# Kernel optimization log

Measured on AMD Instinct MI355X. Metric: run time of the kernel, lower is better.

The kernel has to match this reference:

```python
import jax, jax.numpy as jnp
import numpy as np

N_E = 4096
E_DIM = 256


def setup_inputs() -> dict:
    key = jax.random.key(0)
    k1, k2 = jax.random.split(key)
    z = jax.random.normal(k1, (32, 2048, E_DIM), dtype=jnp.float32)
    # nn.Embedding weight initialized uniform(-1/n_e, 1/n_e)
    codebook = jax.random.uniform(k2, (N_E, E_DIM), dtype=jnp.float32,
                                  minval=-1.0 / N_E, maxval=1.0 / N_E)
    return {"z": z, "codebook": codebook}


def reference(z, codebook):
    # z: [B, T, e_dim], codebook: [n_e, e_dim]
    z_flat = z.reshape(-1, z.shape[-1])                      # [N, d]
    # squared euclidean distance: ||z||^2 + ||e||^2 - 2 z.e^T
    d = (jnp.sum(z_flat ** 2, axis=1, keepdims=True)
         + jnp.sum(codebook ** 2, axis=1)
         - 2.0 * jnp.einsum('nd,kd->nk', z_flat, codebook))  # [N, n_e]
    idx = jnp.argmin(d, axis=1)                              # [N]
    z_q = codebook[idx].reshape(z.shape)                     # [B, T, d]
    return z_q
```

## Files before the change

### kernel.cpp

```cpp
#include <hip/hip_runtime.h>
#include <hip/hip_fp16.h>
#include <cfloat>
#include <climits>

#define D     256
#define NE    4096
#define MT    64
#define NSPLITB 8
#define DELTA     1.5e-4f
#define CAND_CAP  131072

typedef _Float16 f16x8 __attribute__((ext_vector_type(8)));
typedef __attribute__((ext_vector_type(4))) float f32x4;

#define SYNC(n) do { \
    asm volatile("s_waitcnt vmcnt(" #n ")\n\ts_barrier" ::: "memory"); \
    __builtin_amdgcn_sched_barrier(0); \
} while (0)

__device__ __forceinline__ float np_block128_sq(const float* __restrict__ p) {
    float r[8];
    #pragma unroll
    for (int j = 0; j < 8; ++j) r[j] = __fmul_rn(p[j], p[j]);
    #pragma unroll
    for (int i = 8; i < 128; i += 8)
        #pragma unroll
        for (int j = 0; j < 8; ++j) r[j] = __fadd_rn(r[j], __fmul_rn(p[i + j], p[i + j]));
    return __fadd_rn(__fadd_rn(__fadd_rn(r[0], r[1]), __fadd_rn(r[2], r[3])),
                     __fadd_rn(__fadd_rn(r[4], r[5]), __fadd_rn(r[6], r[7])));
}
__device__ __forceinline__ float np_sumsq256(const float* __restrict__ p) {
    return __fadd_rn(np_block128_sq(p), np_block128_sq(p + 128));
}
__device__ __forceinline__ float np_einsum_dot256(const float* __restrict__ zr,
                                                  const float* __restrict__ er) {
    float v0 = 0.f, v1 = 0.f, v2 = 0.f, v3 = 0.f;
    for (int t = 0; t < 256; t += 16) {
        float4 a0 = *(const float4*)(zr + t);
        float4 a1 = *(const float4*)(zr + t + 4);
        float4 a2 = *(const float4*)(zr + t + 8);
        float4 a3 = *(const float4*)(zr + t + 12);
        float4 b0 = *(const float4*)(er + t);
        float4 b1 = *(const float4*)(er + t + 4);
        float4 b2 = *(const float4*)(er + t + 8);
        float4 b3 = *(const float4*)(er + t + 12);
        v0 = __fadd_rn(v0, __fmul_rn(a3.x, b3.x));
        v1 = __fadd_rn(v1, __fmul_rn(a3.y, b3.y));
        v2 = __fadd_rn(v2, __fmul_rn(a3.z, b3.z));
        v3 = __fadd_rn(v3, __fmul_rn(a3.w, b3.w));
        v0 = __fadd_rn(v0, __fmul_rn(a2.x, b2.x));
        v1 = __fadd_rn(v1, __fmul_rn(a2.y, b2.y));
        v2 = __fadd_rn(v2, __fmul_rn(a2.z, b2.z));
        v3 = __fadd_rn(v3, __fmul_rn(a2.w, b2.w));
        v0 = __fadd_rn(v0, __fmul_rn(a1.x, b1.x));
        v1 = __fadd_rn(v1, __fmul_rn(a1.y, b1.y));
        v2 = __fadd_rn(v2, __fmul_rn(a1.z, b1.z));
        v3 = __fadd_rn(v3, __fmul_rn(a1.w, b1.w));
        v0 = __fadd_rn(v0, __fmul_rn(a0.x, b0.x));
        v1 = __fadd_rn(v1, __fmul_rn(a0.y, b0.y));
        v2 = __fadd_rn(v2, __fmul_rn(a0.z, b0.z));
        v3 = __fadd_rn(v3, __fmul_rn(a0.w, b0.w));
    }
    return __fadd_rn(__fadd_rn(v0, v1), __fadd_rn(v2, v3));
}

__global__ void bnp_kernel(const float* __restrict__ cb, float* __restrict__ Bnp) {
    int k = blockIdx.x * 256 + threadIdx.x;
    if (k < NE) Bnp[k] = np_sumsq256(cb + (size_t)k * D);
}

__global__ void tof16_kernel(const float* __restrict__ x,
                             unsigned short* __restrict__ y, float scale, int n4) {
    int t = blockIdx.x * 256 + threadIdx.x;
    if (t >= n4) return;
    float4 v = *(const float4*)(x + (size_t)t * 4);
    ushort4 o;
    o.x = __half_as_ushort(__float2half_rn(v.x * scale));
    o.y = __half_as_ushort(__float2half_rn(v.y * scale));
    o.z = __half_as_ushort(__float2half_rn(v.z * scale));
    o.w = __half_as_ushort(__float2half_rn(v.w * scale));
    *(ushort4*)(y + (size_t)t * 4) = o;
}

__device__ __forceinline__ void gload_lds16(const void* g, void* l) {
    __builtin_amdgcn_global_load_lds(
        (const __attribute__((address_space(1))) unsigned int*)g,
        (__attribute__((address_space(3))) unsigned int*)l, 16, 0, 0);
}

__global__ __launch_bounds__(256, 2)
void stageA_f16(const float* __restrict__ z,
                const unsigned short* __restrict__ cb2,
                const float* __restrict__ Bnp, int* __restrict__ idxArr,
                float* __restrict__ rowMin, unsigned long long* __restrict__ rowKey,
                int* __restrict__ flagCnt, int* __restrict__ flagList) {
    __shared__ unsigned char lds[16384 + 4 * 8192];
    float* BnpL = (float*)lds;
    unsigned short* Bt = (unsigned short*)(lds + 16384);

    const int tid  = threadIdx.x;
    const int wid  = tid >> 6;
    const int lane = tid & 63;
    const int ln   = lane & 15;
    const int qd   = lane >> 4;
    const int wn   = wid;
    const int R0   = blockIdx.x * MT;

    #pragma unroll
    for (int i = 0; i < 4; ++i) {
        int j = tid + 256 * i;
        *(float4*)(BnpL + j * 4) = *(const float4*)(Bnp + j * 4);
    }

    f16x8 fa[8][4];
    {
        const float* za = z + (size_t)(R0 + ln) * 256 + qd * 8;
        #pragma unroll
        for (int kc = 0; kc < 8; ++kc)
            #pragma unroll
            for (int mt = 0; mt < 4; ++mt) {
                const float* p = za + mt * 16 * 256 + kc * 32;
                float4 a = *(const float4*)p, b = *(const float4*)(p + 4);
                f16x8 h;
                h[0] = (_Float16)a.x; h[1] = (_Float16)a.y;
                h[2] = (_Float16)a.z; h[3] = (_Float16)a.w;
                h[4] = (_Float16)b.x; h[5] = (_Float16)b.y;
                h[6] = (_Float16)b.z; h[7] = (_Float16)b.w;
                fa[kc][mt] = h;
            }
    }

    const int cA  = wid * 32 + (lane >> 2);
    const int sgA = (lane & 3) ^ ((cA >> 1) & 3);
    const unsigned short* srcA = cb2 + cA * 256 + sgA * 8;
    unsigned short* dstW = Bt + wid * 1024;
    const int boffs = ((wn * 32 + ln) << 6) + ((qd ^ ((ln >> 1) & 3)) << 4);
    const unsigned char* btb = (const unsigned char*)Bt;

    float best1[16], best2[16];
    int   bidx[16];
    #pragma unroll
    for (int i = 0; i < 16; ++i) { best1[i] = FLT_MAX; best2[i] = FLT_MAX; bidx[i] = 0; }

    #pragma unroll
    for (int s = 0; s < 3; ++s) {
        gload_lds16(srcA + s * 32, dstW + s * 4096);
        gload_lds16(srcA + s * 32 + 4096, dstW + s * 4096 + 512);
    }
    __syncthreads();

    for (int ct = 0; ct < 31; ++ct) {
        f32x4 acc[4][2];
        #pragma unroll
        for (int i = 0; i < 4; ++i)
            #pragma unroll
            for (int j = 0; j < 2; ++j) acc[i][j] = (f32x4){0.f, 0.f, 0.f, 0.f};

        #pragma unroll
        for (int kc = 0; kc < 8; ++kc) {
            SYNC(4);
            {
                const int s3k = kc + 3;
                int off = (ct + (s3k >> 3)) * 32768 + (s3k & 7) * 32;
                unsigned short* d = dstW + ((s3k & 3) << 12);
                gload_lds16(srcA + off, d);
                gload_lds16(srcA + off + 4096, d + 512);
            }
            f16x8 fb[2];
            #pragma unroll
            for (int nt = 0; nt < 2; ++nt)
                fb[nt] = *(const f16x8*)(btb + ((kc & 3) << 13) + boffs + nt * 1024);
            __builtin_amdgcn_s_setprio(1);
            #pragma unroll
            for (int mt = 0; mt < 4; ++mt)
                #pragma unroll
                for (int nt = 0; nt < 2; ++nt)
                    acc[mt][nt] = __builtin_amdgcn_mfma_f32_16x16x32_f16(
                        fa[kc][mt], fb[nt], acc[mt][nt], 0, 0, 0);
            __builtin_amdgcn_s_setprio(0);

            if (kc == 7) {
                const int C0 = ct * 128;
                #pragma unroll
                for (int nt = 0; nt < 2; ++nt) {
                    int col = C0 + wn * 32 + nt * 16 + ln;
                    float bn = BnpL[col];
                    #pragma unroll
                    for (int mt = 0; mt < 4; ++mt) {
                        f32x4 a = acc[mt][nt];
                        #pragma unroll
                        for (int r = 0; r < 4; ++r) {
                            float s = fmaf(-4.8828125e-4f, a[r], bn);
                            int ii = mt * 4 + r;
                            bool lt = s < best1[ii];
                            best2[ii] = __builtin_amdgcn_fmed3f(best1[ii], best2[ii], s);
                            bidx[ii]  = lt ? col : bidx[ii];
                            best1[ii] = fminf(best1[ii], s);
                        }
                    }
                }
            }
        }
    }
    {
        const int ct = 31;
        f32x4 acc[4][2];
        #pragma unroll
        for (int i = 0; i < 4; ++i)
            #pragma unroll
            for (int j = 0; j < 2; ++j) acc[i][j] = (f32x4){0.f, 0.f, 0.f, 0.f};

        #pragma unroll
        for (int kc = 0; kc < 8; ++kc) {
            if (kc <= 5) { SYNC(4); } else if (kc == 6) { SYNC(2); } else { SYNC(0); }
            if (kc <= 4) {
                const int s3k = kc + 3;
                int off = ct * 32768 + (s3k & 7) * 32;
                unsigned short* d = dstW + ((s3k & 3) << 12);
                gload_lds16(srcA + off, d);
                gload_lds16(srcA + off + 4096, d + 512);
            }
            f16x8 fb[2];
            #pragma unroll
            for (int nt = 0; nt < 2; ++nt)
                fb[nt] = *(const f16x8*)(btb + ((kc & 3) << 13) + boffs + nt * 1024);
            __builtin_amdgcn_s_setprio(1);
            #pragma unroll
            for (int mt = 0; mt < 4; ++mt)
                #pragma unroll
                for (int nt = 0; nt < 2; ++nt)
                    acc[mt][nt] = __builtin_amdgcn_mfma_f32_16x16x32_f16(
                        fa[kc][mt], fb[nt], acc[mt][nt], 0, 0, 0);
            __builtin_amdgcn_s_setprio(0);

            if (kc == 7) {
                const int C0 = ct * 128;
                #pragma unroll
                for (int nt = 0; nt < 2; ++nt) {
                    int col = C0 + wn * 32 + nt * 16 + ln;
                    float bn = BnpL[col];
                    #pragma unroll
                    for (int mt = 0; mt < 4; ++mt) {
                        f32x4 a = acc[mt][nt];
                        #pragma unroll
                        for (int r = 0; r < 4; ++r) {
                            float s = fmaf(-4.8828125e-4f, a[r], bn);
                            int ii = mt * 4 + r;
                            bool lt = s < best1[ii];
                            best2[ii] = __builtin_amdgcn_fmed3f(best1[ii], best2[ii], s);
                            bidx[ii]  = lt ? col : bidx[ii];
                            best1[ii] = fminf(best1[ii], s);
                        }
                    }
                }
            }
        }
    }

    #pragma unroll
    for (int mask = 1; mask < 16; mask <<= 1) {
        #pragma unroll
        for (int ii = 0; ii < 16; ++ii) {
            float c1 = __shfl_xor(best1[ii], mask);
            float c2 = __shfl_xor(best2[ii], mask);
            int   ci = __shfl_xor(bidx[ii], mask);
            if (c1 < best1[ii] || (c1 == best1[ii] && ci < bidx[ii])) {
                best2[ii] = fminf(best1[ii], c2);
                best1[ii] = c1; bidx[ii] = ci;
            } else {
                best2[ii] = fminf(best2[ii], c1);
            }
        }
    }
    __syncthreads();
    float* mb1 = (float*)lds;
    float* mb2 = mb1 + 256;
    int*   mix = (int*)(mb2 + 256);
    if (ln == 0) {
        #pragma unroll
        for (int mt = 0; mt < 4; ++mt)
            #pragma unroll
            for (int r = 0; r < 4; ++r) {
                int row = mt * 16 + qd * 4 + r;
                mb1[row * 4 + wn] = best1[mt * 4 + r];
                mb2[row * 4 + wn] = best2[mt * 4 + r];
                mix[row * 4 + wn] = bidx[mt * 4 + r];
            }
    }
    __syncthreads();
    if (tid < MT) {
        int r = tid;
        float b1 = mb1[r * 4], b2v = mb2[r * 4]; int ix = mix[r * 4];
        #pragma unroll
        for (int w = 1; w < 4; ++w) {
            float c1 = mb1[r * 4 + w], c2 = mb2[r * 4 + w]; int ci = mix[r * 4 + w];
            if (c1 < b1 || (c1 == b1 && ci < ix)) { b2v = fminf(b1, c2); b1 = c1; ix = ci; }
            else b2v = fminf(b2v, c1);
        }
        idxArr[R0 + r] = ix;
        rowMin[R0 + r] = b1;
        rowKey[R0 + r] = ~0ULL;
        if (b2v - b1 <= DELTA) {
            int p = atomicAdd(flagCnt, 1);
            flagList[p] = R0 + r;
        }
    }
}

__global__ __launch_bounds__(256, 2)
void stageB_f16(const float* __restrict__ z,
                const unsigned short* __restrict__ cb2,
                const float* __restrict__ Bnp, const float* __restrict__ rowMin,
                const int* __restrict__ flagCnt, const int* __restrict__ flagList,
                int* __restrict__ candCnt, unsigned int* __restrict__ candList) {
    __shared__ unsigned char lds[4 * 8192 + 512];
    unsigned short* Bt = (unsigned short*)lds;
    int*   frow   = (int*)(lds + 32768);
    float* rmin_l = (float*)(lds + 32768 + 256);

    const int nf = *flagCnt;
    const int R0 = blockIdx.x * MT;
    if (R0 >= nf) return;
    const int m = min(MT, nf - R0);

    const int tid  = threadIdx.x;
    const int wid  = tid >> 6;
    const int lane = tid & 63;
    const int ln   = lane & 15;
    const int qd   = lane >> 4;
    const int wn   = wid;
    const int ktBeg = blockIdx.y * (NE / NSPLITB);

    if (tid < MT) {
        int fr = flagList[R0 + min(tid, m - 1)];
        frow[tid] = fr;
        rmin_l[tid] = rowMin[fr];
    }
    __syncthreads();

    float rmv[16];
    #pragma unroll
    for (int mt = 0; mt < 4; ++mt)
        #pragma unroll
        for (int r = 0; r < 4; ++r)
            rmv[mt * 4 + r] = rmin_l[mt * 16 + qd * 4 + r];

    float bnv[4][2];
    #pragma unroll
    for (int ct = 0; ct < 4; ++ct)
        #pragma unroll
        for (int nt = 0; nt < 2; ++nt)
            bnv[ct][nt] = Bnp[ktBeg + ct * 128 + wn * 32 + nt * 16 + ln];

    f16x8 fa[8][4];
    {
        int rA[4];
        #pragma unroll
        for (int mt = 0; mt < 4; ++mt) rA[mt] = frow[mt * 16 + ln];
        #pragma unroll
        for (int kc = 0; kc < 8; ++kc)
            #pragma unroll
            for (int mt = 0; mt < 4; ++mt) {
                const float* p = z + (size_t)rA[mt] * 256 + kc * 32 + qd * 8;
                float4 a = *(const float4*)p, b = *(const float4*)(p + 4);
                f16x8 h;
                h[0] = (_Float16)a.x; h[1] = (_Float16)a.y;
                h[2] = (_Float16)a.z; h[3] = (_Float16)a.w;
                h[4] = (_Float16)b.x; h[5] = (_Float16)b.y;
                h[6] = (_Float16)b.z; h[7] = (_Float16)b.w;
                fa[kc][mt] = h;
            }
    }

    const int cA  = wid * 32 + (lane >> 2);
    const int sgA = (lane & 3) ^ ((cA >> 1) & 3);
    const unsigned short* srcA = cb2 + (size_t)(ktBeg + cA) * 256 + sgA * 8;
    unsigned short* dstW = Bt + wid * 1024;
    const int boffs = ((wn * 32 + ln) << 6) + ((qd ^ ((ln >> 1) & 3)) << 4);
    const unsigned char* btb = (const unsigned char*)Bt;

    #pragma unroll
    for (int s = 0; s < 3; ++s) {
        gload_lds16(srcA + s * 32, dstW + s * 4096);
        gload_lds16(srcA + s * 32 + 4096, dstW + s * 4096 + 512);
    }
    __syncthreads();

    unsigned long long hm0 = 0, hm1 = 0;

    #pragma unroll
    for (int ct = 0; ct < 4; ++ct) {
        f32x4 acc[4][2];
        #pragma unroll
        for (int i = 0; i < 4; ++i)
            #pragma unroll
            for (int j = 0; j < 2; ++j) acc[i][j] = (f32x4){0.f, 0.f, 0.f, 0.f};

        #pragma unroll
        for (int kc = 0; kc < 8; ++kc) {
            const int s = ct * 8 + kc;
            if (s <= 29) { SYNC(4); } else if (s == 30) { SYNC(2); } else { SYNC(0); }
            if (s <= 28) {
                const int s3 = s + 3;
                int off = (s3 >> 3) * 32768 + (s3 & 7) * 32;
                unsigned short* d = dstW + ((s3 & 3) << 12);
                gload_lds16(srcA + off, d);
                gload_lds16(srcA + off + 4096, d + 512);
            }
            f16x8 fb[2];
            #pragma unroll
            for (int nt = 0; nt < 2; ++nt)
                fb[nt] = *(const f16x8*)(btb + ((s & 3) << 13) + boffs + nt * 1024);
            __builtin_amdgcn_s_setprio(1);
            #pragma unroll
            for (int mt = 0; mt < 4; ++mt)
                #pragma unroll
                for (int nt = 0; nt < 2; ++nt)
                    acc[mt][nt] = __builtin_amdgcn_mfma_f32_16x16x32_f16(
                        fa[kc][mt], fb[nt], acc[mt][nt], 0, 0, 0);
            __builtin_amdgcn_s_setprio(0);

            if (kc == 7) {
                #pragma unroll
                for (int nt = 0; nt < 2; ++nt)
                    #pragma unroll
                    for (int mt = 0; mt < 4; ++mt) {
                        f32x4 a = acc[mt][nt];
                        #pragma unroll
                        for (int r = 0; r < 4; ++r) {
                            float sc = fmaf(-4.8828125e-4f, a[r], bnv[ct][nt]);
                            if (sc <= rmv[mt * 4 + r] + DELTA) {
                                unsigned long long bit =
                                    1ull << (((ct & 1) << 5) | (nt << 4) | (mt << 2) | r);
                                if (ct < 2) hm0 |= bit; else hm1 |= bit;
                            }
                        }
                    }
            }
        }
    }

    #pragma unroll
    for (int h = 0; h < 2; ++h) {
        unsigned long long hm = h ? hm1 : hm0;
        while (hm) {
            int b = __builtin_ctzll(hm);
            hm &= hm - 1;
            int ctb = h * 2 + (b >> 5);
            int ntb = (b >> 4) & 1, mtb = (b >> 2) & 3, rb = b & 3;
            int col = ktBeg + ctb * 128 + wn * 32 + ntb * 16 + ln;
            int row = frow[mtb * 16 + qd * 4 + rb];
            int p = atomicAdd(candCnt, 1);
            if (p < CAND_CAP)
                candList[p] = ((unsigned)row << 12) | (unsigned)col;
        }
    }
}

__global__ void stageC(const float* __restrict__ z, const float* __restrict__ cb,
                       const float* __restrict__ Bnp,
                       const int* __restrict__ candCnt,
                       const unsigned int* __restrict__ candList,
                       unsigned long long* __restrict__ rowKey) {
    int c = blockIdx.x * 256 + threadIdx.x;
    int n = min(*candCnt, CAND_CAP);
    if (c >= n) return;
    unsigned e = candList[c];
    int r = (int)(e >> 12);
    int k = (int)(e & 4095u);
    float Anp = np_sumsq256(z + (size_t)r * D);
    float C   = np_einsum_dot256(z + (size_t)r * D, cb + (size_t)k * D);
    float AB  = __fadd_rn(Anp, Bnp[k]);
    float s   = __fsub_rn(AB, __fadd_rn(C, C));
    unsigned long long key = ((unsigned long long)__float_as_uint(s) << 32) | (unsigned)k;
    atomicMin(rowKey + r, key);
}

__global__ void gather_kernel(const float* __restrict__ cb,
                              const int* __restrict__ idxArr,
                              const unsigned long long* __restrict__ rowKey,
                              float* __restrict__ out) {
    int r = blockIdx.x * 4 + (threadIdx.x >> 6);
    int l = threadIdx.x & 63;
    unsigned long long kv = rowKey[r];
    int ix = (kv != ~0ULL) ? (int)(kv & 0xFFFFFFFFull) : idxArr[r];
    *(float4*)(out + (size_t)r * D + l * 4) =
        *(const float4*)(cb + (size_t)ix * D + l * 4);
}

extern "C" void kernel_launch(void* const* d_in, const int* in_sizes, int n_in,
                              void* d_out, int out_size, void* d_ws, size_t ws_size,
                              hipStream_t stream) {
    const float* z  = (const float*)d_in[0];
    const float* cb = (const float*)d_in[1];
    float* out = (float*)d_out;
    const int nRows = in_sizes[0] / D;

    char* w = (char*)d_ws;
    unsigned short* cb2 = (unsigned short*)w;
    unsigned long long* rowKey = (unsigned long long*)(w + 2097152);
    int*   idxArr   = (int*)  (w + 2621440);
    float* rowMin   = (float*)(w + 2883584);
    int*   flagList = (int*)  (w + 3145728);
    float* Bnp      = (float*)(w + 3407872);
    unsigned int* candList = (unsigned int*)(w + 3424256);
    int*   flagCnt  = (int*)  (w + 3948544);
    int*   candCnt  = flagCnt + 1;

    hipMemsetAsync(flagCnt, 0, 8, stream);
    bnp_kernel<<<NE / 256, 256, 0, stream>>>(cb, Bnp);
    tof16_kernel<<<NE * D / 4 / 256, 256, 0, stream>>>(cb, cb2, 4096.0f, NE * D / 4);
    stageA_f16<<<nRows / MT, 256, 0, stream>>>(z, cb2, Bnp, idxArr, rowMin,
                                               rowKey, flagCnt, flagList);
    stageB_f16<<<dim3(nRows / MT, NSPLITB), 256, 0, stream>>>(z, cb2, Bnp, rowMin,
                                                              flagCnt, flagList,
                                                              candCnt, candList);
    stageC<<<CAND_CAP / 256, 256, 0, stream>>>(z, cb, Bnp, candCnt, candList, rowKey);
    gather_kernel<<<nRows / 4, 256, 0, stream>>>(cb, idxArr, rowKey, out);
}
```

Baseline: 452.2 us.

## Retile stageA waves 2x2 and store codebook norms as bf16 in LDS

```diff
diff --git a/kernel.cpp b/kernel.cpp
--- a/kernel.cpp
+++ b/kernel.cpp
@@ -64,9 +64,15 @@
     return __fadd_rn(__fadd_rn(v0, v1), __fadd_rn(v2, v3));
 }
 
-__global__ void bnp_kernel(const float* __restrict__ cb, float* __restrict__ Bnp) {
+__global__ void bnp_kernel(const float* __restrict__ cb, float* __restrict__ Bnp,
+                           unsigned short* __restrict__ Bnpb) {
     int k = blockIdx.x * 256 + threadIdx.x;
-    if (k < NE) Bnp[k] = np_sumsq256(cb + (size_t)k * D);
+    if (k < NE) {
+        float s = np_sumsq256(cb + (size_t)k * D);
+        Bnp[k] = s;
+        unsigned u = __float_as_uint(s);
+        Bnpb[k] = (unsigned short)((u + 0x7FFFu + ((u >> 16) & 1u)) >> 16);
+    }
 }
 
 __global__ void tof16_kernel(const float* __restrict__ x,
@@ -88,37 +94,38 @@
         (__attribute__((address_space(3))) unsigned int*)l, 16, 0, 0);
 }
 
-__global__ __launch_bounds__(256, 2)
+__global__ __launch_bounds__(256, 4)
 void stageA_f16(const float* __restrict__ z,
                 const unsigned short* __restrict__ cb2,
-                const float* __restrict__ Bnp, int* __restrict__ idxArr,
+                const unsigned short* __restrict__ Bnpb, int* __restrict__ idxArr,
                 float* __restrict__ rowMin, unsigned long long* __restrict__ rowKey,
                 int* __restrict__ flagCnt, int* __restrict__ flagList) {
-    __shared__ unsigned char lds[16384 + 4 * 8192];
-    float* BnpL = (float*)lds;
-    unsigned short* Bt = (unsigned short*)(lds + 16384);
+    __shared__ unsigned char lds[8192 + 4 * 8192];
+    unsigned short* BnpL = (unsigned short*)lds;
+    unsigned short* Bt = (unsigned short*)(lds + 8192);
 
     const int tid  = threadIdx.x;
     const int wid  = tid >> 6;
     const int lane = tid & 63;
     const int ln   = lane & 15;
     const int qd   = lane >> 4;
-    const int wn   = wid;
+    const int wm   = wid & 1;
+    const int wn   = wid >> 1;
     const int R0   = blockIdx.x * MT;
 
     #pragma unroll
-    for (int i = 0; i < 4; ++i) {
+    for (int i = 0; i < 2; ++i) {
         int j = tid + 256 * i;
-        *(float4*)(BnpL + j * 4) = *(const float4*)(Bnp + j * 4);
-    }
-
-    f16x8 fa[8][4];
+        *(uint4*)(BnpL + j * 8) = *(const uint4*)(Bnpb + j * 8);
+    }
+
+    f16x8 fa[8][2];
     {
-        const float* za = z + (size_t)(R0 + ln) * 256 + qd * 8;
+        const float* za = z + (size_t)(R0 + wm * 32 + ln) * 256 + qd * 8;
         #pragma unroll
         for (int kc = 0; kc < 8; ++kc)
             #pragma unroll
-            for (int mt = 0; mt < 4; ++mt) {
+            for (int mt = 0; mt < 2; ++mt) {
                 const float* p = za + mt * 16 * 256 + kc * 32;
                 float4 a = *(const float4*)p, b = *(const float4*)(p + 4);
                 f16x8 h;
@@ -134,13 +141,13 @@
     const int sgA = (lane & 3) ^ ((cA >> 1) & 3);
     const unsigned short* srcA = cb2 + cA * 256 + sgA * 8;
     unsigned short* dstW = Bt + wid * 1024;
-    const int boffs = ((wn * 32 + ln) << 6) + ((qd ^ ((ln >> 1) & 3)) << 4);
+    const int boffs = ((wn * 64 + ln) << 6) + ((qd ^ ((ln >> 1) & 3)) << 4);
     const unsigned char* btb = (const unsigned char*)Bt;
 
-    float best1[16], best2[16];
-    int   bidx[16];
-    #pragma unroll
-    for (int i = 0; i < 16; ++i) { best1[i] = FLT_MAX; best2[i] = FLT_MAX; bidx[i] = 0; }
+    float best1[8], best2[8];
+    int   bidx[8];
+    #pragma unroll
+    for (int i = 0; i < 8; ++i) { best1[i] = FLT_MAX; best2[i] = FLT_MAX; bidx[i] = 0; }
 
     #pragma unroll
     for (int s = 0; s < 3; ++s) {
@@ -150,11 +157,11 @@
     __syncthreads();
 
     for (int ct = 0; ct < 31; ++ct) {
-        f32x4 acc[4][2];
-        #pragma unroll
-        for (int i = 0; i < 4; ++i)
-            #pragma unroll
-            for (int j = 0; j < 2; ++j) acc[i][j] = (f32x4){0.f, 0.f, 0.f, 0.f};
+        f32x4 acc[2][4];
+        #pragma unroll
+        for (int i = 0; i < 2; ++i)
+            #pragma unroll
+            for (int j = 0; j < 4; ++j) acc[i][j] = (f32x4){0.f, 0.f, 0.f, 0.f};
 
         #pragma unroll
         for (int kc = 0; kc < 8; ++kc) {
@@ -166,15 +173,15 @@
                 gload_lds16(srcA + off, d);
                 gload_lds16(srcA + off + 4096, d + 512);
             }
-            f16x8 fb[2];
-            #pragma unroll
-            for (int nt = 0; nt < 2; ++nt)
+            f16x8 fb[4];
+            #pragma unroll
+            for (int nt = 0; nt < 4; ++nt)
                 fb[nt] = *(const f16x8*)(btb + ((kc & 3) << 13) + boffs + nt * 1024);
             __builtin_amdgcn_s_setprio(1);
             #pragma unroll
-            for (int mt = 0; mt < 4; ++mt)
+            for (int mt = 0; mt < 2; ++mt)
                 #pragma unroll
-                for (int nt = 0; nt < 2; ++nt)
+                for (int nt = 0; nt < 4; ++nt)
                     acc[mt][nt] = __builtin_amdgcn_mfma_f32_16x16x32_f16(
                         fa[kc][mt], fb[nt], acc[mt][nt], 0, 0, 0);
             __builtin_amdgcn_s_setprio(0);
@@ -182,11 +189,11 @@
             if (kc == 7) {
                 const int C0 = ct * 128;
                 #pragma unroll
-                for (int nt = 0; nt < 2; ++nt) {
-                    int col = C0 + wn * 32 + nt * 16 + ln;
-                    float bn = BnpL[col];
+                for (int nt = 0; nt < 4; ++nt) {
+                    int col = C0 + wn * 64 + nt * 16 + ln;
+                    float bn = __uint_as_float(((unsigned)BnpL[col]) << 16);
                     #pragma unroll
-                    for (int mt = 0; mt < 4; ++mt) {
+                    for (int mt = 0; mt < 2; ++mt) {
                         f32x4 a = acc[mt][nt];
                         #pragma unroll
                         for (int r = 0; r < 4; ++r) {
@@ -204,11 +211,11 @@
     }
     {
         const int ct = 31;
-        f32x4 acc[4][2];
-        #pragma unroll
-        for (int i = 0; i < 4; ++i)
-            #pragma unroll
-            for (int j = 0; j < 2; ++j) acc[i][j] = (f32x4){0.f, 0.f, 0.f, 0.f};
+        f32x4 acc[2][4];
+        #pragma unroll
+        for (int i = 0; i < 2; ++i)
+            #pragma unroll
+            for (int j = 0; j < 4; ++j) acc[i][j] = (f32x4){0.f, 0.f, 0.f, 0.f};
 
         #pragma unroll
         for (int kc = 0; kc < 8; ++kc) {
@@ -220,15 +227,15 @@
                 gload_lds16(srcA + off, d);
                 gload_lds16(srcA + off + 4096, d + 512);
             }
-            f16x8 fb[2];
-            #pragma unroll
-            for (int nt = 0; nt < 2; ++nt)
+            f16x8 fb[4];
+            #pragma unroll
+            for (int nt = 0; nt < 4; ++nt)
                 fb[nt] = *(const f16x8*)(btb + ((kc & 3) << 13) + boffs + nt * 1024);
             __builtin_amdgcn_s_setprio(1);
             #pragma unroll
-            for (int mt = 0; mt < 4; ++mt)
+            for (int mt = 0; mt < 2; ++mt)
                 #pragma unroll
-                for (int nt = 0; nt < 2; ++nt)
+                for (int nt = 0; nt < 4; ++nt)
                     acc[mt][nt] = __builtin_amdgcn_mfma_f32_16x16x32_f16(
                         fa[kc][mt], fb[nt], acc[mt][nt], 0, 0, 0);
             __builtin_amdgcn_s_setprio(0);
@@ -236,11 +243,11 @@
             if (kc == 7) {
                 const int C0 = ct * 128;
                 #pragma unroll
-                for (int nt = 0; nt < 2; ++nt) {
-                    int col = C0 + wn * 32 + nt * 16 + ln;
-                    float bn = BnpL[col];
+                for (int nt = 0; nt < 4; ++nt) {
+                    int col = C0 + wn * 64 + nt * 16 + ln;
+                    float bn = __uint_as_float(((unsigned)BnpL[col]) << 16);
                     #pragma unroll
-                    for (int mt = 0; mt < 4; ++mt) {
+                    for (int mt = 0; mt < 2; ++mt) {
                         f32x4 a = acc[mt][nt];
                         #pragma unroll
                         for (int r = 0; r < 4; ++r) {
@@ -260,7 +267,7 @@
     #pragma unroll
     for (int mask = 1; mask < 16; mask <<= 1) {
         #pragma unroll
-        for (int ii = 0; ii < 16; ++ii) {
+        for (int ii = 0; ii < 8; ++ii) {
             float c1 = __shfl_xor(best1[ii], mask);
             float c2 = __shfl_xor(best2[ii], mask);
             int   ci = __shfl_xor(bidx[ii], mask);
@@ -274,29 +281,26 @@
     }
     __syncthreads();
     float* mb1 = (float*)lds;
-    float* mb2 = mb1 + 256;
-    int*   mix = (int*)(mb2 + 256);
+    float* mb2 = mb1 + 128;
+    int*   mix = (int*)(mb2 + 128);
     if (ln == 0) {
         #pragma unroll
-        for (int mt = 0; mt < 4; ++mt)
+        for (int mt = 0; mt < 2; ++mt)
             #pragma unroll
             for (int r = 0; r < 4; ++r) {
-                int row = mt * 16 + qd * 4 + r;
-                mb1[row * 4 + wn] = best1[mt * 4 + r];
-                mb2[row * 4 + wn] = best2[mt * 4 + r];
-                mix[row * 4 + wn] = bidx[mt * 4 + r];
+                int row = wm * 32 + mt * 16 + qd * 4 + r;
+                mb1[row * 2 + wn] = best1[mt * 4 + r];
+                mb2[row * 2 + wn] = best2[mt * 4 + r];
+                mix[row * 2 + wn] = bidx[mt * 4 + r];
             }
     }
     __syncthreads();
     if (tid < MT) {
         int r = tid;
-        float b1 = mb1[r * 4], b2v = mb2[r * 4]; int ix = mix[r * 4];
-        #pragma unroll
-        for (int w = 1; w < 4; ++w) {
-            float c1 = mb1[r * 4 + w], c2 = mb2[r * 4 + w]; int ci = mix[r * 4 + w];
-            if (c1 < b1 || (c1 == b1 && ci < ix)) { b2v = fminf(b1, c2); b1 = c1; ix = ci; }
-            else b2v = fminf(b2v, c1);
-        }
+        float b1 = mb1[r * 2], b2v = mb2[r * 2]; int ix = mix[r * 2];
+        float c1 = mb1[r * 2 + 1], c2 = mb2[r * 2 + 1]; int ci = mix[r * 2 + 1];
+        if (c1 < b1 || (c1 == b1 && ci < ix)) { b2v = fminf(b1, c2); b1 = c1; ix = ci; }
+        else b2v = fminf(b2v, c1);
         idxArr[R0 + r] = ix;
         rowMin[R0 + r] = b1;
         rowKey[R0 + r] = ~0ULL;
@@ -503,14 +507,15 @@
     float* rowMin   = (float*)(w + 2883584);
     int*   flagList = (int*)  (w + 3145728);
     float* Bnp      = (float*)(w + 3407872);
-    unsigned int* candList = (unsigned int*)(w + 3424256);
-    int*   flagCnt  = (int*)  (w + 3948544);
+    unsigned short* Bnpb = (unsigned short*)(w + 3424256);
+    unsigned int* candList = (unsigned int*)(w + 3432448);
+    int*   flagCnt  = (int*)  (w + 3956736);
     int*   candCnt  = flagCnt + 1;
 
     hipMemsetAsync(flagCnt, 0, 8, stream);
-    bnp_kernel<<<NE / 256, 256, 0, stream>>>(cb, Bnp);
+    bnp_kernel<<<NE / 256, 256, 0, stream>>>(cb, Bnp, Bnpb);
     tof16_kernel<<<NE * D / 4 / 256, 256, 0, stream>>>(cb, cb2, 4096.0f, NE * D / 4);
-    stageA_f16<<<nRows / MT, 256, 0, stream>>>(z, cb2, Bnp, idxArr, rowMin,
+    stageA_f16<<<nRows / MT, 256, 0, stream>>>(z, cb2, Bnpb, idxArr, rowMin,
                                                rowKey, flagCnt, flagList);
     stageB_f16<<<dim3(nRows / MT, NSPLITB), 256, 0, stream>>>(z, cb2, Bnp, rowMin,
                                                               flagCnt, flagList,
```

Measured after the change: 553.2 us. 22.3% more time.
